# Performance work log

Hardware: AMD Instinct MI355X
Metric: run time of the kernel (lower is better)

## Reference

```python
import jax, jax.numpy as jnp
import numpy as np

B, S, D, H = 8, 1024, 256, 8
DH = D // H
NEG = -1e32


def setup_inputs() -> dict:
    key = jax.random.key(0)
    ks = jax.random.split(key, 8)
    scale = 1.0 / np.sqrt(D)
    return {
        "q": jax.random.normal(ks[0], (B, S, D), jnp.float32),
        "k": jax.random.normal(ks[1], (B, S, D), jnp.float32),
        "v": jax.random.normal(ks[2], (B, S, D), jnp.float32),
        "mask": jnp.tril(jnp.ones((1, 1, S, S), dtype=bool)),
        "Wq": jax.random.normal(ks[3], (D, D), jnp.float32) * scale,
        "bq": jnp.zeros((D,), jnp.float32),
        "Wv": jax.random.normal(ks[4], (D, D), jnp.float32) * scale,
        "bv": jnp.zeros((D,), jnp.float32),
        "Wo": jax.random.normal(ks[5], (D, D), jnp.float32) * scale,
        "bo": jnp.zeros((D,), jnp.float32),
        "gammas": jax.random.normal(ks[6], (H, 1, 1), jnp.float32) * 0.1,
    }


def reference(q, k, v, mask, Wq, bq, Wv, bv, Wo, bo, gammas):
    def split_heads(x):  # [B,S,D] -> [B,H,S,DH]
        return x.reshape(B, S, H, DH).transpose(0, 2, 1, 3)

    # key_query_same=True: key projection shares query weights
    qh = split_heads(q @ Wq.T + bq)
    kh = split_heads(k @ Wq.T + bq)
    vh = split_heads(v @ Wv.T + bv)

    scores = jnp.einsum('bhqd,bhkd->bhqk', qh, kh) / jnp.sqrt(jnp.float32(DH))

    # distance-decay effect (computed on detached softmax of masked scores)
    sp = jax.nn.softmax(jnp.where(mask, scores, NEG), axis=-1)
    distcum = jnp.cumsum(sp, axis=-1)                      # [B,H,S,S]
    disttot = jnp.sum(sp, axis=-1, keepdims=True)          # [B,H,S,1]
    pos = jnp.abs(jnp.arange(S)[None, :] - jnp.arange(S)[:, None]).astype(jnp.float32)
    dist = jnp.sqrt(jnp.clip((disttot - distcum) * pos[None, None], 0.0, None))
    dist = jax.lax.stop_gradient(dist)

    g = -jnp.abs(gammas)[None]                             # [1,H,1,1]
    total_effect = jnp.clip(jnp.exp(g * dist), 1e-5, 1e5)

    scores = scores * total_effect
    scores = jax.nn.softmax(jnp.where(mask, scores, NEG), axis=-1)

    out = jnp.einsum('bhqk,bhkd->bhqd', scores, vh)
    concat = out.transpose(0, 2, 1, 3).reshape(B, S, D)
    output = concat @ Wo.T + bo
    return output, scores
```

## Files before the change

### kernel.cpp

```cpp
#include <hip/hip_runtime.h>
#include <hip/hip_fp16.h>
#include <math.h>

constexpr int Bsz = 8, Ssz = 1024, Dsz = 256, Hn = 8, DHn = 32;
constexpr int SST = 1160;

typedef __attribute__((ext_vector_type(8))) short short8;
typedef __attribute__((ext_vector_type(4))) float floatx4;

#define DEV static __device__ __forceinline__

DEV short f2bf(float f) {
  union { float f; unsigned u; } x; x.f = f;
  return (short)((x.u + 0x7fffu + ((x.u >> 16) & 1u)) >> 16);
}
DEV short f2h(float f) {
  __half h = __float2half(f);
  return *(short*)&h;
}
DEV unsigned bfpk(float lo, float hi) {
  unsigned r;
  asm("v_cvt_pk_bf16_f32 %0, %1, %2" : "=v"(r) : "v"(lo), "v"(hi));
  return r;
}
DEV float ex2(float x) {
#if __has_builtin(__builtin_amdgcn_exp2f)
  return __builtin_amdgcn_exp2f(x);
#else
  return __expf(x * 0.69314718055994531f);
#endif
}
DEV float wsum(float v) {
#pragma unroll
  for (int off = 32; off > 0; off >>= 1) v += __shfl_xor(v, off, 64);
  return v;
}

__global__ __launch_bounds__(256) void cvt_wfrag(const float* __restrict__ Wq,
                                                 const float* __restrict__ Wv,
                                                 const float* __restrict__ Wo,
                                                 short* __restrict__ dst) {
  const int which = blockIdx.y;
  const float* W = (which == 0) ? Wq : (which == 1) ? Wv : Wo;
  const int t = blockIdx.x * 256 + threadIdx.x;
  const int ln = t & 63, nt = (t >> 6) & 15, kblk = t >> 10;
  const float* src = W + (size_t)(nt * 16 + (ln & 15)) * 256 + kblk * 32 + (ln >> 4) * 8;
  const float4 a = *(const float4*)src;
  const float4 b = *(const float4*)(src + 4);
  const float tmp[8] = {a.x, a.y, a.z, a.w, b.x, b.y, b.z, b.w};
  short8 s;
#pragma unroll
  for (int j = 0; j < 8; ++j) s[j] = f2bf(tmp[j]);
  *(short8*)(dst + ((size_t)which << 16) + (size_t)t * 8) = s;
}

__global__ __launch_bounds__(256, 4) void proj_qkv2(
    const float* __restrict__ qi, const float* __restrict__ ki, const float* __restrict__ vi,
    const short* __restrict__ Wfrag, const float* __restrict__ bq, const float* __restrict__ bv,
    short* __restrict__ qh, short* __restrict__ kh, short* __restrict__ vt) {
  __shared__ short Xs[32 * 80];
  const int which = blockIdx.y;
  const float* X = (which == 0) ? qi : (which == 1) ? ki : vi;
  const short* Wf = Wfrag + ((which == 2) ? (1 << 16) : 0);
  const float* bias = (which == 2) ? bv : bq;
  const int tid = threadIdx.x, ln = tid & 63, w = tid >> 6;
  const int lm = ln & 15, qq = ln >> 4;
  const int bm = blockIdx.x;
  const float* Xb = X + (size_t)bm * 32 * 256;
  floatx4 acc[2][4] = {};

  for (int k0 = 0; k0 < 4; ++k0) {
    __syncthreads();
    {
      const int row = tid >> 3, cg = tid & 7;
#pragma unroll
      for (int i = 0; i < 2; ++i) {
        const float4 f = *(const float4*)(Xb + (size_t)row * 256 + k0 * 64 + cg * 8 + i * 4);
        short4 s; s.x = f2bf(f.x); s.y = f2bf(f.y); s.z = f2bf(f.z); s.w = f2bf(f.w);
        *(short4*)(Xs + row * 80 + (cg ^ (row & 7)) * 8 + i * 4) = s;
      }
    }
    __syncthreads();
#pragma unroll
    for (int ks = 0; ks < 2; ++ks) {
      const int kblk = k0 * 2 + ks;
      short8 a[2], b[4];
#pragma unroll
      for (int mt = 0; mt < 2; ++mt) {
        const int row = mt * 16 + lm;
        a[mt] = *(const short8*)(Xs + row * 80 + (((ks * 4 + qq)) ^ (row & 7)) * 8);
      }
#pragma unroll
      for (int nt = 0; nt < 4; ++nt)
        b[nt] = *(const short8*)(Wf + ((size_t)(kblk * 16 + w * 4 + nt) * 64 + ln) * 8);
#pragma unroll
      for (int mt = 0; mt < 2; ++mt)
#pragma unroll
        for (int nt = 0; nt < 4; ++nt)
          acc[mt][nt] = __builtin_amdgcn_mfma_f32_16x16x32_bf16(a[mt], b[nt], acc[mt][nt], 0, 0, 0);
    }
  }

#pragma unroll
  for (int mt = 0; mt < 2; ++mt) {
#pragma unroll
    for (int nt = 0; nt < 4; ++nt) {
      const int n = w * 64 + nt * 16 + lm;
      const float bval = bias[n];
      const int m0 = bm * 32 + mt * 16 + qq * 4;
      const int h = n >> 5, dh = n & 31;
      if (which <= 1) {
        short* dst = (which == 0) ? qh : kh;
#pragma unroll
        for (int r = 0; r < 4; ++r) {
          const int m = m0 + r, b_ = m >> 10, s = m & 1023;
          dst[(((size_t)(b_ * Hn + h) << 10) + s) * DHn + dh] = f2bf(acc[mt][nt][r] + bval);
        }
      } else {
        const int b_ = m0 >> 10, s0 = m0 & 1023;
        short4 pk;
        pk.x = f2bf(acc[mt][nt][0] + bval);
        pk.y = f2bf(acc[mt][nt][1] + bval);
        pk.z = f2bf(acc[mt][nt][2] + bval);
        pk.w = f2bf(acc[mt][nt][3] + bval);
        *(short4*)(vt + ((size_t)((b_ * Hn + h) * DHn + dh) << 10) + s0) = pk;
      }
    }
  }
}

__global__ __launch_bounds__(256, 4) void proj_out2(
    const short* __restrict__ oc, const short* __restrict__ Wfrag,
    const float* __restrict__ bo, float* __restrict__ out) {
  __shared__ short Xs[32 * 80];
  const short* Wf = Wfrag + (2 << 16);
  const int tid = threadIdx.x, ln = tid & 63, w = tid >> 6;
  const int lm = ln & 15, qq = ln >> 4;
  const int bm = blockIdx.x;
  const short* Xb = oc + (size_t)bm * 32 * 256;
  floatx4 acc[2][4] = {};

  for (int k0 = 0; k0 < 4; ++k0) {
    __syncthreads();
    {
      const int row = tid >> 3, cg = tid & 7;
      const short8 s = *(const short8*)(Xb + (size_t)row * 256 + k0 * 64 + cg * 8);
      *(short8*)(Xs + row * 80 + (cg ^ (row & 7)) * 8) = s;
    }
    __syncthreads();
#pragma unroll
    for (int ks = 0; ks < 2; ++ks) {
      const int kblk = k0 * 2 + ks;
      short8 a[2], b[4];
#pragma unroll
      for (int mt = 0; mt < 2; ++mt) {
        const int row = mt * 16 + lm;
        a[mt] = *(const short8*)(Xs + row * 80 + (((ks * 4 + qq)) ^ (row & 7)) * 8);
      }
#pragma unroll
      for (int nt = 0; nt < 4; ++nt)
        b[nt] = *(const short8*)(Wf + ((size_t)(kblk * 16 + w * 4 + nt) * 64 + ln) * 8);
#pragma unroll
      for (int mt = 0; mt < 2; ++mt)
#pragma unroll
        for (int nt = 0; nt < 4; ++nt)
          acc[mt][nt] = __builtin_amdgcn_mfma_f32_16x16x32_bf16(a[mt], b[nt], acc[mt][nt], 0, 0, 0);
    }
  }
#pragma unroll
  for (int mt = 0; mt < 2; ++mt)
#pragma unroll
    for (int nt = 0; nt < 4; ++nt) {
      const int n = w * 64 + nt * 16 + lm;
      const float bval = bo[n];
      const int m0 = bm * 32 + mt * 16 + qq * 4;
#pragma unroll
      for (int r = 0; r < 4; ++r)
        __builtin_nontemporal_store(acc[mt][nt][r] + bval, out + (size_t)(m0 + r) * 256 + n);
    }
}

template <int NP>
DEV void phase2(short* ss, float* shead, int row0, int w, int ln, float g2) {
  const int c0 = ln * 4;
  for (int rr = 0; rr < 4; ++rr) {
    const int m = w * 4 + rr;
    const int irow = row0 + m;
    short* srow = ss + m * SST;

    float sv[NP * 4], e[NP * 4], ls[NP];

#pragma unroll
    for (int p = 0; p < NP; ++p) {
      const uint2 u = *(const uint2*)(srow + p * 256 + c0);
      const float2 f0 = __half22float2(*(const __half2*)&u.x);
      const float2 f1 = __half22float2(*(const __half2*)&u.y);
      sv[p * 4 + 0] = f0.x; sv[p * 4 + 1] = f0.y;
      sv[p * 4 + 2] = f1.x; sv[p * 4 + 3] = f1.y;
      float l = 0.f;
#pragma unroll
      for (int j = 0; j < 4; ++j) {
        float ex = ex2(sv[p * 4 + j]);
        if (p == NP - 1)
          ex = (p * 256 + c0 + j <= irow) ? ex : 0.f;
        e[p * 4 + j] = ex;
        l += ex;
      }
      ls[p] = l;
    }

    float incl[NP];
#pragma unroll
    for (int p = 0; p < NP; ++p) incl[p] = ls[p];
#pragma unroll
    for (int off = 1; off < 64; off <<= 1) {
#pragma unroll
      for (int p = 0; p < NP; ++p) {
        const float y = __shfl_up(incl[p], off, 64);
        if (ln >= off) incl[p] += y;
      }
    }
    float excl[NP], Z = 0.f;
#pragma unroll
    for (int p = 0; p < NP; ++p) {
      excl[p] = Z + incl[p] - ls[p];
      Z += __shfl(incl[p], 63, 64);
    }
    const float invZ = 1.f / Z;

    float ls2 = 0.f;
#pragma unroll
    for (int p = 0; p < NP; ++p) {
      float cum = excl[p];
      float pos = (float)(irow - (p * 256 + c0));
#pragma unroll
      for (int j = 0; j < 4; ++j) {
        cum += e[p * 4 + j];
        const float tail = 1.f - cum * invZ;
        const float dist = sqrtf(__builtin_fabsf(tail * pos));
        const float eff = fmaxf(ex2(g2 * dist), 1e-5f);
        float x = ex2(sv[p * 4 + j] * eff);
        if (p == NP - 1)
          x = (p * 256 + c0 + j <= irow) ? x : 0.f;
        e[p * 4 + j] = x;
        ls2 += x;
        pos -= 1.f;
      }
    }
    const float i2 = 1.f / wsum(ls2);

    float* grow = shead + (size_t)irow * Ssz;
#pragma unroll
    for (int p = 0; p < NP; ++p) {
      floatx4 o;
      o.x = e[p * 4 + 0] * i2; o.y = e[p * 4 + 1] * i2;
      o.z = e[p * 4 + 2] * i2; o.w = e[p * 4 + 3] * i2;
      __builtin_nontemporal_store(o, (floatx4*)(grow + p * 256 + c0));
      uint2 pk;
      pk.x = bfpk(o.x, o.y);
      pk.y = bfpk(o.z, o.w);
      *(uint2*)(srow + p * 256 + c0) = pk;
    }
  }
}

__global__ __launch_bounds__(256, 4) void attn_kernel(
    const short* __restrict__ qh, const short* __restrict__ kh,
    const short* __restrict__ vt, const float* __restrict__ gammas,
    float* __restrict__ scores_out, short* __restrict__ oc) {
  __shared__ short ss[16 * SST];

  const int tid = threadIdx.x, ln = tid & 63, w = tid >> 6;
  const int lm = ln & 15, qq = ln >> 4;
  const int bh = blockIdx.x >> 6;
  const int row0 = (63 - (blockIdx.x & 63)) << 4;
  const int h = bh & 7, b = bh >> 3;
  const float scaleL2e = 0.17677669529663687f * 1.4426950408889634f;
  const float g2 = -fabsf(gammas[h]) * 1.4426950408889634f;

  const short* qhead = qh + (size_t)bh * Ssz * DHn;
  const short* khead = kh + (size_t)bh * Ssz * DHn;
  const short* vhead = vt + (size_t)bh * DHn * Ssz;
  float* shead = scores_out + ((size_t)bh << 20);

  const short8 qa = *(const short8*)(qhead + (row0 + lm) * DHn + qq * 8);

  const int ntile = (row0 >> 4) + 1;
  for (int t = w; t < ntile; t += 4) {
    const int n0 = t * 16;
    const short8 kb = *(const short8*)(khead + (n0 + lm) * DHn + qq * 8);
    floatx4 c = {0.f, 0.f, 0.f, 0.f};
    c = __builtin_amdgcn_mfma_f32_16x16x32_bf16(qa, kb, c, 0, 0, 0);
#pragma unroll
    for (int r = 0; r < 4; ++r)
      ss[(qq * 4 + r) * SST + n0 + lm] = f2h(c[r] * scaleL2e);
  }
  __syncthreads();

  const int NPc = (row0 >> 8) + 1;
  switch (NPc) {
    case 1: phase2<1>(ss, shead, row0, w, ln, g2); break;
    case 2: phase2<2>(ss, shead, row0, w, ln, g2); break;
    case 3: phase2<3>(ss, shead, row0, w, ln, g2); break;
    default: phase2<4>(ss, shead, row0, w, ln, g2); break;
  }

  if (NPc < 4) {
    const floatx4 z4 = {0.f, 0.f, 0.f, 0.f};
    for (int r = 0; r < 16; ++r) {
      float* grow = shead + (size_t)(row0 + r) * Ssz + NPc * 256;
      for (int i = tid; i < (4 - NPc) * 64; i += 256)
        __builtin_nontemporal_store(z4, ((floatx4*)grow) + i);
    }
  }
  __syncthreads();

  floatx4 o0 = {0.f, 0.f, 0.f, 0.f}, o1 = {0.f, 0.f, 0.f, 0.f};
  const int nkt = (row0 >> 5) + 1;
  for (int kt = w; kt < nkt; kt += 4) {
    const int k0 = kt * 32;
    const short8 av = *(const short8*)(ss + lm * SST + k0 + qq * 8);
    const short8 b0 = *(const short8*)(vhead + (lm << 10) + k0 + qq * 8);
    const short8 b1 = *(const short8*)(vhead + ((16 + lm) << 10) + k0 + qq * 8);
    o0 = __builtin_amdgcn_mfma_f32_16x16x32_bf16(av, b0, o0, 0, 0, 0);
    o1 = __builtin_amdgcn_mfma_f32_16x16x32_bf16(av, b1, o1, 0, 0, 0);
  }
  __syncthreads();
  float* red = (float*)ss;
#pragma unroll
  for (int r = 0; r < 4; ++r) {
    red[(w * 16 + qq * 4 + r) * 32 + lm] = o0[r];
    red[(w * 16 + qq * 4 + r) * 32 + 16 + lm] = o1[r];
  }
  __syncthreads();
  {
    const int m = tid >> 4, n = tid & 15;
    float a0 = 0.f, a1 = 0.f;
#pragma unroll
    for (int wv = 0; wv < 4; ++wv) {
      a0 += red[(wv * 16 + m) * 32 + n];
      a1 += red[(wv * 16 + m) * 32 + 16 + n];
    }
    const size_t row = ((size_t)b << 10) + row0 + m;
    oc[row * Dsz + h * DHn + n] = f2bf(a0);
    oc[row * Dsz + h * DHn + 16 + n] = f2bf(a1);
  }
}

extern "C" void kernel_launch(void* const* d_in, const int* in_sizes, int n_in,
                              void* d_out, int out_size, void* d_ws, size_t ws_size,
                              hipStream_t stream) {
  const float* q  = (const float*)d_in[0];
  const float* k  = (const float*)d_in[1];
  const float* v  = (const float*)d_in[2];
  const float* Wq = (const float*)d_in[4];
  const float* bq = (const float*)d_in[5];
  const float* Wv = (const float*)d_in[6];
  const float* bv = (const float*)d_in[7];
  const float* Wo = (const float*)d_in[8];
  const float* bo = (const float*)d_in[9];
  const float* gm = (const float*)d_in[10];

  float* out    = (float*)d_out;
  float* scores = out + (size_t)Bsz * Ssz * Dsz;

  const size_t Q = (size_t)Bsz * Hn * Ssz * DHn;
  short* qh = (short*)d_ws;
  short* kh = qh + Q;
  short* vt = kh + Q;
  short* oc = vt + Q;
  short* Wf = oc + Q;

  const dim3 blk(256);
  hipLaunchKernelGGL(cvt_wfrag, dim3(32, 3), blk, 0, stream, Wq, Wv, Wo, Wf);
  hipLaunchKernelGGL(proj_qkv2, dim3(256, 3), blk, 0, stream,
                     q, k, v, Wf, bq, bv, qh, kh, vt);
  hipLaunchKernelGGL(attn_kernel, dim3(Bsz * Hn * (Ssz / 16)), blk, 0, stream,
                     qh, kh, vt, gm, scores, oc);
  hipLaunchKernelGGL(proj_out2, dim3(256), blk, 0, stream, oc, Wf, bo, out);
}
```

Measured before the change: 358.2 us.

## Swizzle score LDS layout, shrink registers, fuse zero-fill, dual-accumulate PV

```diff
diff --git a/kernel.cpp b/kernel.cpp
--- a/kernel.cpp
+++ b/kernel.cpp
@@ -3,12 +3,15 @@
 #include <math.h>
 
 constexpr int Bsz = 8, Ssz = 1024, Dsz = 256, Hn = 8, DHn = 32;
-constexpr int SST = 1160;
+constexpr int SST = 1024;
 
 typedef __attribute__((ext_vector_type(8))) short short8;
 typedef __attribute__((ext_vector_type(4))) float floatx4;
+typedef __attribute__((ext_vector_type(2))) float floatx2;
 
 #define DEV static __device__ __forceinline__
+
+DEV int swz(int row, int col) { return col ^ ((row & 7) << 3); }
 
 DEV short f2bf(float f) {
   union { float f; unsigned u; } x; x.f = f;
@@ -181,32 +184,31 @@
 }
 
 template <int NP>
-DEV void phase2(short* ss, float* shead, int row0, int w, int ln, float g2) {
+DEV void phase2(short* ss, float* shead, int row0, int w, int ln, float gsq) {
   const int c0 = ln * 4;
   for (int rr = 0; rr < 4; ++rr) {
     const int m = w * 4 + rr;
     const int irow = row0 + m;
     short* srow = ss + m * SST;
 
-    float sv[NP * 4], e[NP * 4], ls[NP];
+    floatx2 e01[NP], e23[NP];
+    float ls[NP];
 
 #pragma unroll
     for (int p = 0; p < NP; ++p) {
-      const uint2 u = *(const uint2*)(srow + p * 256 + c0);
+      const uint2 u = *(const uint2*)(srow + swz(m, p * 256 + c0));
       const float2 f0 = __half22float2(*(const __half2*)&u.x);
       const float2 f1 = __half22float2(*(const __half2*)&u.y);
-      sv[p * 4 + 0] = f0.x; sv[p * 4 + 1] = f0.y;
-      sv[p * 4 + 2] = f1.x; sv[p * 4 + 3] = f1.y;
-      float l = 0.f;
-#pragma unroll
-      for (int j = 0; j < 4; ++j) {
-        float ex = ex2(sv[p * 4 + j]);
-        if (p == NP - 1)
-          ex = (p * 256 + c0 + j <= irow) ? ex : 0.f;
-        e[p * 4 + j] = ex;
-        l += ex;
-      }
-      ls[p] = l;
+      float e0 = ex2(f0.x), e1 = ex2(f0.y), e2 = ex2(f1.x), e3 = ex2(f1.y);
+      if (p == NP - 1) {
+        const int cb = p * 256 + c0;
+        e0 = (cb + 0 <= irow) ? e0 : 0.f;
+        e1 = (cb + 1 <= irow) ? e1 : 0.f;
+        e2 = (cb + 2 <= irow) ? e2 : 0.f;
+        e3 = (cb + 3 <= irow) ? e3 : 0.f;
+      }
+      e01[p].x = e0; e01[p].y = e1; e23[p].x = e2; e23[p].y = e3;
+      ls[p] = (e0 + e1) + (e2 + e3);
     }
 
     float incl[NP];
@@ -231,40 +233,53 @@
     float ls2 = 0.f;
 #pragma unroll
     for (int p = 0; p < NP; ++p) {
+      const uint2 u = *(const uint2*)(srow + swz(m, p * 256 + c0));
+      const float2 f0 = __half22float2(*(const __half2*)&u.x);
+      const float2 f1 = __half22float2(*(const __half2*)&u.y);
+      const float tv[4] = {f0.x, f0.y, f1.x, f1.y};
+      const float ev[4] = {e01[p].x, e01[p].y, e23[p].x, e23[p].y};
       float cum = excl[p];
-      float pos = (float)(irow - (p * 256 + c0));
+      float pos = gsq * (float)(irow - (p * 256 + c0));
+      float xv[4];
 #pragma unroll
       for (int j = 0; j < 4; ++j) {
-        cum += e[p * 4 + j];
+        cum += ev[j];
         const float tail = 1.f - cum * invZ;
-        const float dist = sqrtf(__builtin_fabsf(tail * pos));
-        const float eff = fmaxf(ex2(g2 * dist), 1e-5f);
-        float x = ex2(sv[p * 4 + j] * eff);
+        const float d = sqrtf(__builtin_fabsf(tail * pos));
+        const float eff = fmaxf(ex2(-d), 1e-5f);
+        float x = ex2(tv[j] * eff);
         if (p == NP - 1)
           x = (p * 256 + c0 + j <= irow) ? x : 0.f;
-        e[p * 4 + j] = x;
+        xv[j] = x;
         ls2 += x;
-        pos -= 1.f;
-      }
+        pos -= gsq;
+      }
+      e01[p].x = xv[0]; e01[p].y = xv[1];
+      e23[p].x = xv[2]; e23[p].y = xv[3];
     }
     const float i2 = 1.f / wsum(ls2);
 
     float* grow = shead + (size_t)irow * Ssz;
-#pragma unroll
-    for (int p = 0; p < NP; ++p) {
+    const floatx4 z4 = {0.f, 0.f, 0.f, 0.f};
+#pragma unroll
+    for (int p = 0; p < 4; ++p) {
+      if (p >= NP) {
+        __builtin_nontemporal_store(z4, (floatx4*)(grow + p * 256 + c0));
+        continue;
+      }
       floatx4 o;
-      o.x = e[p * 4 + 0] * i2; o.y = e[p * 4 + 1] * i2;
-      o.z = e[p * 4 + 2] * i2; o.w = e[p * 4 + 3] * i2;
+      o.x = e01[p].x * i2; o.y = e01[p].y * i2;
+      o.z = e23[p].x * i2; o.w = e23[p].y * i2;
       __builtin_nontemporal_store(o, (floatx4*)(grow + p * 256 + c0));
       uint2 pk;
       pk.x = bfpk(o.x, o.y);
       pk.y = bfpk(o.z, o.w);
-      *(uint2*)(srow + p * 256 + c0) = pk;
-    }
-  }
-}
-
-__global__ __launch_bounds__(256, 4) void attn_kernel(
+      *(uint2*)(srow + swz(m, p * 256 + c0)) = pk;
+    }
+  }
+}
+
+__global__ __launch_bounds__(256, 5) void attn_kernel(
     const short* __restrict__ qh, const short* __restrict__ kh,
     const short* __restrict__ vt, const float* __restrict__ gammas,
     float* __restrict__ scores_out, short* __restrict__ oc) {
@@ -277,6 +292,7 @@
   const int h = bh & 7, b = bh >> 3;
   const float scaleL2e = 0.17677669529663687f * 1.4426950408889634f;
   const float g2 = -fabsf(gammas[h]) * 1.4426950408889634f;
+  const float gsq = g2 * g2;
 
   const short* qhead = qh + (size_t)bh * Ssz * DHn;
   const short* khead = kh + (size_t)bh * Ssz * DHn;
@@ -292,39 +308,54 @@
     floatx4 c = {0.f, 0.f, 0.f, 0.f};
     c = __builtin_amdgcn_mfma_f32_16x16x32_bf16(qa, kb, c, 0, 0, 0);
 #pragma unroll
-    for (int r = 0; r < 4; ++r)
-      ss[(qq * 4 + r) * SST + n0 + lm] = f2h(c[r] * scaleL2e);
+    for (int r = 0; r < 4; ++r) {
+      const int row = qq * 4 + r;
+      ss[row * SST + swz(row, n0 + lm)] = f2h(c[r] * scaleL2e);
+    }
   }
   __syncthreads();
 
   const int NPc = (row0 >> 8) + 1;
   switch (NPc) {
-    case 1: phase2<1>(ss, shead, row0, w, ln, g2); break;
-    case 2: phase2<2>(ss, shead, row0, w, ln, g2); break;
-    case 3: phase2<3>(ss, shead, row0, w, ln, g2); break;
-    default: phase2<4>(ss, shead, row0, w, ln, g2); break;
-  }
-
-  if (NPc < 4) {
-    const floatx4 z4 = {0.f, 0.f, 0.f, 0.f};
-    for (int r = 0; r < 16; ++r) {
-      float* grow = shead + (size_t)(row0 + r) * Ssz + NPc * 256;
-      for (int i = tid; i < (4 - NPc) * 64; i += 256)
-        __builtin_nontemporal_store(z4, ((floatx4*)grow) + i);
-    }
+    case 1: phase2<1>(ss, shead, row0, w, ln, gsq); break;
+    case 2: phase2<2>(ss, shead, row0, w, ln, gsq); break;
+    case 3: phase2<3>(ss, shead, row0, w, ln, gsq); break;
+    default: phase2<4>(ss, shead, row0, w, ln, gsq); break;
   }
   __syncthreads();
 
   floatx4 o0 = {0.f, 0.f, 0.f, 0.f}, o1 = {0.f, 0.f, 0.f, 0.f};
+  floatx4 p0 = {0.f, 0.f, 0.f, 0.f}, p1 = {0.f, 0.f, 0.f, 0.f};
   const int nkt = (row0 >> 5) + 1;
-  for (int kt = w; kt < nkt; kt += 4) {
+  int kt = w;
+  for (; kt + 4 < nkt; kt += 8) {
+    {
+      const int k0 = kt * 32;
+      const short8 av = *(const short8*)(ss + lm * SST + swz(lm, k0 + qq * 8));
+      const short8 b0 = *(const short8*)(vhead + (lm << 10) + k0 + qq * 8);
+      const short8 b1 = *(const short8*)(vhead + ((16 + lm) << 10) + k0 + qq * 8);
+      o0 = __builtin_amdgcn_mfma_f32_16x16x32_bf16(av, b0, o0, 0, 0, 0);
+      o1 = __builtin_amdgcn_mfma_f32_16x16x32_bf16(av, b1, o1, 0, 0, 0);
+    }
+    {
+      const int k0 = (kt + 4) * 32;
+      const short8 av = *(const short8*)(ss + lm * SST + swz(lm, k0 + qq * 8));
+      const short8 b0 = *(const short8*)(vhead + (lm << 10) + k0 + qq * 8);
+      const short8 b1 = *(const short8*)(vhead + ((16 + lm) << 10) + k0 + qq * 8);
+      p0 = __builtin_amdgcn_mfma_f32_16x16x32_bf16(av, b0, p0, 0, 0, 0);
+      p1 = __builtin_amdgcn_mfma_f32_16x16x32_bf16(av, b1, p1, 0, 0, 0);
+    }
+  }
+  if (kt < nkt) {
     const int k0 = kt * 32;
-    const short8 av = *(const short8*)(ss + lm * SST + k0 + qq * 8);
+    const short8 av = *(const short8*)(ss + lm * SST + swz(lm, k0 + qq * 8));
     const short8 b0 = *(const short8*)(vhead + (lm << 10) + k0 + qq * 8);
     const short8 b1 = *(const short8*)(vhead + ((16 + lm) << 10) + k0 + qq * 8);
     o0 = __builtin_amdgcn_mfma_f32_16x16x32_bf16(av, b0, o0, 0, 0, 0);
     o1 = __builtin_amdgcn_mfma_f32_16x16x32_bf16(av, b1, o1, 0, 0, 0);
   }
+  o0 = o0 + p0;
+  o1 = o1 + p1;
   __syncthreads();
   float* red = (float*)ss;
 #pragma unroll
```

Result: no change. 360.9 us (+0.8%).
